# Kernel optimization log

Measured on AMD Instinct MI355X. Metric: run time of the kernel, lower is better.

The kernel has to match this reference:

```python
import jax, jax.numpy as jnp
import numpy as np

B, F, T, C, G = 2, 2048, 750, 20, 3
K = int(T * 0.125)  # top-k for score_pre


def _conv1d(x, w, b=None, pad=0):
    # x: (N, Cin, L), w: (Cout, Cin, k)
    out = jax.lax.conv_general_dilated(x, w, (1,), [(pad, pad)],
                                       dimension_numbers=('NCH', 'OIH', 'NCH'))
    return out if b is None else out + b[None, :, None]


def _base(x, w1, b1, w2, b2):
    # BaseModule: two k=3 convs with LeakyReLU(0.01); dropout = identity (eval)
    h = jax.nn.leaky_relu(_conv1d(x, w1, b1, pad=1))
    h = jax.nn.leaky_relu(_conv1d(h, w2, b2, pad=1))
    return h


def _post_cls(feat_agg, w1, b1, w2, b2, wc, batch, g):
    # feat_agg: (batch*C, F, g) -> BaseModule -> grouped 1x1 classifier -> mean over g
    h = _base(feat_agg, w1, b1, w2, b2)            # (batch*C, 2048, g)
    h = h.reshape(batch, C, 2048, g)
    score = jnp.einsum('bckg,ck->bcg', h, wc[:, :, 0])  # grouped conv1d, groups=C
    return score.mean(axis=2)                       # (batch, C)


def setup_inputs():
    key = jax.random.key(0)
    ks = jax.random.split(key, 8)
    s = 0.02
    x = jax.random.normal(ks[0], (B, F, T), jnp.float32)
    w1 = jax.random.normal(ks[1], (2048, F, 3), jnp.float32) * s
    b1 = jnp.zeros((2048,), jnp.float32)
    w2 = jax.random.normal(ks[2], (2048, 2048, 3), jnp.float32) * s
    b2 = jnp.zeros((2048,), jnp.float32)
    wc = jax.random.normal(ks[3], (C, 2048, 1), jnp.float32) * s   # classifier, no bias
    watt = jax.random.normal(ks[4], (C, C, 1), jnp.float32) * s    # attention 1x1 conv
    batt = jnp.zeros((C,), jnp.float32)
    cls_label = (jax.random.uniform(ks[5], (B, C)) < 0.15).astype(jnp.int32)
    cls_label = cls_label.at[:, 0].set(1)  # guarantee >=1 gt class per video
    return {'x': x, 'w1': w1, 'b1': b1, 'w2': w2, 'b2': b2, 'wc': wc,
            'watt': watt, 'batt': batt, 'cls_label': cls_label,
            'groups': G, 'is_train': 1}


def reference(x, w1, b1, w2, b2, wc, watt, batt, cls_label, groups, is_train):
    g = groups
    Tg = T // g
    seq_cas = _conv1d(_base(x, w1, b1, w2, b2), wc)           # (B, C, T)
    score_pre = jax.lax.top_k(seq_cas, K)[0].mean(axis=2)     # (B, C)
    wa = jax.nn.sigmoid(_conv1d(seq_cas, watt, batt))         # (B, C, T) attention weights

    # _agg_feature: strided slice t = j*g + i  <=>  reshape T -> (Tg, g), group idx last
    xg = x.reshape(B, F, Tg, g)
    wag = wa.reshape(B, C, Tg, g)
    feat_agg = jnp.einsum('bcjg,bfjg->bcfg', wag, xg).reshape(B * C, F, g)
    score_post = _post_cls(feat_agg, w1, b1, w2, b2, wc, B, g)  # (B, C)

    if is_train:
        # background stream, vectorized over (batch, suppressed class c) with masking
        wbg = (1.0 - wa).reshape(B, C, Tg, g)
        # tiny intermediate (B,C,C,Tg,g), then contract with features
        ww = jnp.einsum('bajg,bcjg->bcajg', wag, wbg)
        agg = jnp.einsum('bcajg,bfjg->bcafg', ww, xg).reshape(B * C * C, F, g)
        sc = _post_cls(agg, w1, b1, w2, b2, wc, B * C, g).reshape(B, C, C)  # [b, suppressed c, class a]
        m = cls_label.astype(score_post.dtype)                 # (B, C) multi-hot
        ngt = jnp.maximum(m.sum(axis=1, keepdims=True), 1.0)
        collect = jnp.einsum('bc,bca->ba', m, sc) / ngt        # mean over gt classes
        diag = jnp.diagonal(sc, axis1=1, axis2=2)              # sc[b, j, j]
        collect = jnp.where(m > 0, diag, collect)              # overwrite gt entries
        score_agg = jax.nn.softmax(jnp.concatenate([score_post, collect], axis=1), axis=1)
        return (score_pre, score_post, score_agg)
    else:
        return (jax.nn.softmax(score_pre, axis=1), seq_cas)
```

## Files before the change

kernel.cpp:

```cpp
#include <hip/hip_runtime.h>
#include <math.h>

namespace {
constexpr int kF = 2048;
constexpr int kT = 750;
constexpr int kC = 20;
constexpr int kTop = 93;
}

typedef __bf16 bf16x8 __attribute__((ext_vector_type(8)));
typedef float f32x4 __attribute__((ext_vector_type(4)));

__device__ __forceinline__ ushort f2bf(float f) {
  uint u = __builtin_bit_cast(uint, f);
  uint r = u + 0x7FFFu + ((u >> 16) & 1u);
  return (ushort)(r >> 16);
}
__device__ __forceinline__ float bf2f(ushort u) {
  return __builtin_bit_cast(float, ((uint)u) << 16);
}
__device__ __forceinline__ float leaky(float v) { return v > 0.f ? v : 0.01f * v; }

__device__ __forceinline__ void gload_lds16(const ushort* g, ushort* l) {
  __builtin_amdgcn_global_load_lds(
      (const __attribute__((address_space(1))) void*)g,
      (__attribute__((address_space(3))) void*)l, 16, 0, 0);
}

__global__ void build_list_kernel(const int* __restrict__ lbl,
                                  int4* __restrict__ meta, int* __restrict__ cnt) {
  if (threadIdx.x != 0) return;
  int n = 0;
  for (int b = 0; b < 2; ++b) {
    cnt[4 + b] = n;
    for (int c = 0; c < kC; ++c) { meta[n] = make_int4(b, c, c, 1); ++n; }
    int nb0 = n;
    for (int c = 0; c < kC; ++c)
      for (int a = 0; a < kC; ++a)
        if (lbl[b * kC + c] > 0 || c == a) { meta[n] = make_int4(b, c, a, 0); ++n; }
    cnt[6 + b] = (n - cnt[4 + b]);
    (void)nb0;
  }
  cnt[0] = n;
  cnt[1] = n * 3;
  cnt[2] = 1500;
  cnt[3] = 0;
}

__global__ __launch_bounds__(256) void convert_w_kernel(
    const float* __restrict__ w1, const float* __restrict__ w2,
    ushort* __restrict__ Wt1, ushort* __restrict__ Wt2,
    ushort* __restrict__ zpage) {
  const int co = blockIdx.x;
  const float* w = (blockIdx.y == 0) ? w1 : w2;
  ushort* Wt = (blockIdx.y == 0) ? Wt1 : Wt2;
  const int ci0 = threadIdx.x * 8;
  float v[24];
  const float4* p = (const float4*)(w + (size_t)co * 6144 + ci0 * 3);
#pragma unroll
  for (int s = 0; s < 6; ++s) {
    float4 f = p[s];
    v[s * 4 + 0] = f.x; v[s * 4 + 1] = f.y; v[s * 4 + 2] = f.z; v[s * 4 + 3] = f.w;
  }
#pragma unroll
  for (int tap = 0; tap < 3; ++tap) {
    ushort o[8];
#pragma unroll
    for (int j = 0; j < 8; ++j) o[j] = f2bf(v[j * 3 + tap]);
    ushort4 a = {o[0], o[1], o[2], o[3]}, b = {o[4], o[5], o[6], o[7]};
    ushort4* q = (ushort4*)(Wt + (size_t)tap * kF * kF + (size_t)co * kF + ci0);
    q[0] = a; q[1] = b;
  }
  if (blockIdx.x == 0 && blockIdx.y == 0) {
    ((float4*)zpage)[threadIdx.x] = (float4){0.f, 0.f, 0.f, 0.f};
  }
}

__global__ __launch_bounds__(256) void convert_kernel(
    const float* __restrict__ src, ushort* __restrict__ dst, int n) {
  int i = (blockIdx.x * 256 + threadIdx.x) * 4;
  if (i + 3 < n) {
    float4 f = *(const float4*)(src + i);
    ushort4 o;
    o.x = f2bf(f.x); o.y = f2bf(f.y); o.z = f2bf(f.z); o.w = f2bf(f.w);
    *(ushort4*)(dst + i) = o;
  } else {
    for (; i < n; ++i) dst[i] = f2bf(src[i]);
  }
}

__global__ __launch_bounds__(256) void transpose_kernel(
    const float* __restrict__ x, ushort* __restrict__ xTt) {
  __shared__ float tile[64][65];
  const int b = blockIdx.z;
  const int t0 = blockIdx.x * 64, f0 = blockIdx.y * 64;
  const int tx = threadIdx.x & 63, ty4 = threadIdx.x >> 6;
#pragma unroll
  for (int i = 0; i < 16; ++i) {
    int lf = ty4 + i * 4;
    int t = t0 + tx;
    tile[lf][tx] = (t < kT) ? x[((size_t)b * kF + f0 + lf) * kT + t] : 0.f;
  }
  __syncthreads();
#pragma unroll
  for (int i = 0; i < 16; ++i) {
    int lt = ty4 + i * 4;
    int t = t0 + lt;
    if (t < kT)
      xTt[(size_t)(b * kT + t) * kF + f0 + tx] = f2bf(tile[tx][lt]);
  }
}

__global__ __launch_bounds__(256) void xj_kernel(
    const float* __restrict__ x, ushort* __restrict__ xJ) {
  const int bid = blockIdx.x;
  const int b = bid >> 11, f = bid & 2047;
  __shared__ float buf[768];
  const float* xr = x + ((size_t)b * kF + f) * kT;
  for (int t = threadIdx.x; t < kT; t += 256) buf[t] = xr[t];
  __syncthreads();
  const int j = threadIdx.x;
#pragma unroll
  for (int g = 0; g < 3; ++g) {
    float v = (j < 250) ? buf[j * 3 + g] : 0.f;
    xJ[(((size_t)(b * 3 + g) * kF + f) << 8) + j] = f2bf(v);
  }
}

__global__ __launch_bounds__(256) void ww_build_kernel(
    const float* __restrict__ wab, const int4* __restrict__ meta,
    const int* __restrict__ cnt, ushort* __restrict__ W2) {
  const int bg = blockIdx.x;
  const int b = bg / 3, g = bg % 3;
  const int r0 = blockIdx.y * 32;
  const int nb = cnt[6 + b], boff = cnt[4 + b];
  if (r0 >= nb) return;
  __shared__ float ws[kC][256];
  for (int i = threadIdx.x; i < kC * 250; i += 256) {
    int c = i / 250, j = i % 250;
    ws[c][j] = wab[(size_t)(b * kC + c) * kT + j * 3 + g];
  }
  __syncthreads();
  ushort* Wb = W2 + (size_t)bg * 512 * 256;
  const int j = threadIdx.x;
  for (int rr = 0; rr < 32; ++rr) {
    int r = r0 + rr;
    if (r >= nb) break;
    int4 m = meta[boff + r];
    float v = 0.f;
    if (j < 250)
      v = m.w ? ws[m.y][j] : ws[m.z][j] * (1.f - ws[m.y][j]);
    Wb[(size_t)r * 256 + j] = f2bf(v);
  }
}

__global__ __launch_bounds__(256) void ww_gemm_kernel(
    const ushort* __restrict__ xJ, const ushort* __restrict__ W2,
    const int* __restrict__ cnt, ushort* __restrict__ FeatY) {
  const int bg = blockIdx.z;
  const int b = bg / 3, g = bg % 3;
  const int nb = cnt[6 + b], boff = cnt[4 + b];
  const int s0 = blockIdx.x * 128;
  if (s0 >= nb) return;
  __shared__ ushort sA[2][128 * 64];
  __shared__ ushort sB[2][128 * 64];
  const int tid = threadIdx.x;
  const int w = tid >> 6, lane = tid & 63;
  const int wm = w >> 1, wn = w & 1;
  const int f0 = blockIdx.y * 128;
  const ushort* A = xJ + ((size_t)bg * kF << 8);
  const ushort* Bp = W2 + (size_t)bg * 512 * 256;
  const int srow = lane >> 3;
  const int selem = ((lane & 7) ^ srow) * 8;
  f32x4 acc[4][4];
#pragma unroll
  for (int i = 0; i < 4; ++i)
#pragma unroll
    for (int j = 0; j < 4; ++j) acc[i][j] = (f32x4){0.f, 0.f, 0.f, 0.f};

  auto STAGE = [&](int buf, int kt) {
    const int kin = kt * 64;
#pragma unroll
    for (int i = 0; i < 4; ++i) {
      int r = (w * 4 + i) * 8 + srow;
      gload_lds16(A + (size_t)(f0 + r) * 256 + kin + selem,
                  &sA[buf][(w * 4 + i) * 512]);
    }
#pragma unroll
    for (int i = 0; i < 4; ++i) {
      int r = (w * 4 + i) * 8 + srow;
      gload_lds16(Bp + (size_t)(s0 + r) * 256 + kin + selem,
                  &sB[buf][(w * 4 + i) * 512]);
    }
  };

  STAGE(0, 0);
  asm volatile("s_waitcnt vmcnt(0)" ::: "memory");
  __builtin_amdgcn_s_barrier();

  int cur = 0;
  for (int kt = 0; kt < 4; ++kt) {
    if (kt + 1 < 4) STAGE(cur ^ 1, kt + 1);
#pragma unroll
    for (int ksub = 0; ksub < 2; ++ksub) {
      bf16x8 af[4], bfv[4];
      const int rlow = lane & 7;
#pragma unroll
      for (int fm = 0; fm < 4; ++fm) {
        int row = wm * 64 + fm * 16 + (lane & 15);
        int c16 = (ksub * 4 + (lane >> 4)) ^ rlow;
        af[fm] = *(const bf16x8*)&sA[cur][row * 64 + c16 * 8];
      }
#pragma unroll
      for (int fn = 0; fn < 4; ++fn) {
        int row = wn * 64 + fn * 16 + (lane & 15);
        int c16 = (ksub * 4 + (lane >> 4)) ^ rlow;
        bfv[fn] = *(const bf16x8*)&sB[cur][row * 64 + c16 * 8];
      }
#pragma unroll
      for (int fm = 0; fm < 4; ++fm)
#pragma unroll
        for (int fn = 0; fn < 4; ++fn)
          acc[fm][fn] = __builtin_amdgcn_mfma_f32_16x16x32_bf16(
              af[fm], bfv[fn], acc[fm][fn], 0, 0, 0);
    }
    asm volatile("s_waitcnt vmcnt(0)" ::: "memory");
    __builtin_amdgcn_s_barrier();
    cur ^= 1;
  }

#pragma unroll
  for (int fm = 0; fm < 4; ++fm) {
#pragma unroll
    for (int fn = 0; fn < 4; ++fn) {
      int s = s0 + wn * 64 + fn * 16 + (lane & 15);
      if (s >= nb) continue;
      int row = f0 + wm * 64 + fm * 16 + ((lane >> 4) << 2);
      ushort4 o;
      o.x = f2bf(acc[fm][fn][0]);
      o.y = f2bf(acc[fm][fn][1]);
      o.z = f2bf(acc[fm][fn][2]);
      o.w = f2bf(acc[fm][fn][3]);
      *(ushort4*)&FeatY[(size_t)((boff + s) * 3 + g) * kF + row] = o;
    }
  }
}

template <int L>
__global__ __launch_bounds__(512, 1) void gemm_conv_kernel(
    const ushort* __restrict__ A, const ushort* __restrict__ B,
    const ushort* __restrict__ zpage, ushort* __restrict__ Cpart,
    const int* __restrict__ ncp, int NP, int ktn_base, int ktrem) {
  extern __shared__ ushort lds[];
  const int nc = *ncp;
  const int tid = threadIdx.x;
  const int wid = tid >> 6, lane = tid & 63;
  const int wr = wid >> 2, wc = wid & 3;
  const int gx = gridDim.x, gy = gridDim.y;
  const int nwg = gx * gy * gridDim.z;
  const int h = blockIdx.x + gx * (blockIdx.y + gy * blockIdx.z);
  const int lgc = (h & 7) * (nwg >> 3) + (h >> 3);
  const int bx = lgc % gx;
  const int byz = lgc / gx;
  const int co0 = (byz % gy) * 256;
  const int col0 = bx * 256;
  if (col0 >= nc) return;
  const int z = byz / gy;
  const int kt0 = z * ktn_base + (z < ktrem ? z : ktrem);
  const int ktn = ktn_base + (z < ktrem ? 1 : 0);
  const int ktend = kt0 + ktn;

  const int pofs = lane >> 3;
  const int lin_s = (lane & 7) ^ pofs;
  const int mofs = 2 * pofs + (lin_s >> 2);
  const int qseg = (lin_s & 3) * 8;
  const int l15 = lane & 15;
  const int seg8 = ((((l15 & 1) << 2) + (lane >> 4)) ^ (l15 >> 1)) * 8;
  const int off_rl = (l15 >> 1) * 64 + seg8;

  f32x4 acc[8][4];
#pragma unroll
  for (int i = 0; i < 8; ++i)
#pragma unroll
    for (int j = 0; j < 4; ++j) acc[i][j] = (f32x4){0.f, 0.f, 0.f, 0.f};

  auto STAGE_A = [&](int buf, int kt) {
    const int tap = kt >> 6;
    const int kin = (kt & 63) * 32;
    const size_t abase = (size_t)tap * kF * kF + kin + qseg;
#pragma unroll
    for (int l = 0; l < 2; ++l) {
      int m = l * 128 + wid * 16 + mofs;
      gload_lds16(A + abase + (size_t)(co0 + m) * kF,
                  &lds[buf * 16384 + l * 4096 + wid * 512]);
    }
  };
  auto STAGE_B = [&](int buf, int kt) {
    const int tap = kt >> 6;
    const int kin = (kt & 63) * 32;
#pragma unroll
    for (int l = 0; l < 2; ++l) {
      int m = l * 128 + wid * 16 + mofs;
      int col = col0 + m;
      int t = col - (col / L) * L;
      int tt = t + tap - 1;
      const ushort* src = (col < nc && tt >= 0 && tt < L)
          ? B + (size_t)(col + tap - 1) * kF + kin + qseg
          : zpage + qseg;
      gload_lds16(src, &lds[buf * 16384 + 8192 + l * 4096 + wid * 512]);
    }
  };

  STAGE_A(kt0 & 3, kt0);           STAGE_B(kt0 & 3, kt0);
  STAGE_A((kt0 + 1) & 3, kt0 + 1); STAGE_B((kt0 + 1) & 3, kt0 + 1);
  STAGE_A((kt0 + 2) & 3, kt0 + 2); STAGE_B((kt0 + 2) & 3, kt0 + 2);
  asm volatile("s_waitcnt vmcnt(8)" ::: "memory");
  __builtin_amdgcn_s_barrier();
  __builtin_amdgcn_sched_barrier(0);

  for (int kt = kt0; kt < ktend; ++kt) {
    const int buf = kt & 3;
    const int ts = (kt + 3 < ktend) ? kt + 3 : ktend - 1;
    const int bufs = ts & 3;
    const ushort* bb = &lds[buf * 16384];
    bf16x8 bfv[4], af[4];
    STAGE_A(bufs, ts);
#pragma unroll
    for (int fn = 0; fn < 4; ++fn)
      bfv[fn] = *(const bf16x8*)&bb[8192 + wc * 2048 + fn * 512 + off_rl];
#pragma unroll
    for (int fm = 0; fm < 4; ++fm)
      af[fm] = *(const bf16x8*)&bb[wr * 4096 + fm * 512 + off_rl];
    asm volatile("s_waitcnt lgkmcnt(0)" ::: "memory");
    __builtin_amdgcn_sched_barrier(0);
    __builtin_amdgcn_s_setprio(1);
#pragma unroll
    for (int fm = 0; fm < 4; ++fm)
#pragma unroll
      for (int fn = 0; fn < 4; ++fn)
        acc[fm][fn] = __builtin_amdgcn_mfma_f32_16x16x32_bf16(
            af[fm], bfv[fn], acc[fm][fn], 0, 0, 0);
    __builtin_amdgcn_s_setprio(0);
    STAGE_B(bufs, ts);
#pragma unroll
    for (int fm = 0; fm < 4; ++fm)
      af[fm] = *(const bf16x8*)&bb[wr * 4096 + (fm + 4) * 512 + off_rl];
    asm volatile("s_waitcnt lgkmcnt(0)" ::: "memory");
    __builtin_amdgcn_sched_barrier(0);
    __builtin_amdgcn_s_setprio(1);
#pragma unroll
    for (int fm = 0; fm < 4; ++fm)
#pragma unroll
      for (int fn = 0; fn < 4; ++fn)
        acc[fm + 4][fn] = __builtin_amdgcn_mfma_f32_16x16x32_bf16(
            af[fm], bfv[fn], acc[fm + 4][fn], 0, 0, 0);
    __builtin_amdgcn_s_setprio(0);
    asm volatile("s_waitcnt vmcnt(8)" ::: "memory");
    __builtin_amdgcn_s_barrier();
    __builtin_amdgcn_sched_barrier(0);
  }

  ushort* Cz = Cpart + (size_t)z * NP * kF;
#pragma unroll
  for (int fm = 0; fm < 8; ++fm) {
#pragma unroll
    for (int fn = 0; fn < 4; ++fn) {
      int col = col0 + wc * 64 + fn * 16 + l15;
      int row = co0 + wr * 128 + fm * 16 + ((lane >> 4) << 2);
      ushort4 o;
      o.x = f2bf(acc[fm][fn][0]);
      o.y = f2bf(acc[fm][fn][1]);
      o.z = f2bf(acc[fm][fn][2]);
      o.w = f2bf(acc[fm][fn][3]);
      *(ushort4*)&Cz[(size_t)col * kF + row] = o;
    }
  }
}

__global__ __launch_bounds__(256) void reduce_kernel(
    const ushort* __restrict__ Cpart, const float* __restrict__ bias,
    ushort* __restrict__ Y, const int* __restrict__ ncp, int NP, int S) {
  const int col = blockIdx.x;
  if (col >= *ncp) return;
  const int row0 = threadIdx.x * 8;
  float s[8] = {};
  for (int z = 0; z < S; ++z) {
    const ushort* p = &Cpart[((size_t)z * NP + col) * kF + row0];
    ushort4 a = *(const ushort4*)p;
    ushort4 b = *(const ushort4*)(p + 4);
    s[0] += bf2f(a.x); s[1] += bf2f(a.y); s[2] += bf2f(a.z); s[3] += bf2f(a.w);
    s[4] += bf2f(b.x); s[5] += bf2f(b.y); s[6] += bf2f(b.z); s[7] += bf2f(b.w);
  }
  float4 bv0 = *(const float4*)&bias[row0];
  float4 bv1 = *(const float4*)&bias[row0 + 4];
  ushort4 o0, o1;
  o0.x = f2bf(leaky(s[0] + bv0.x)); o0.y = f2bf(leaky(s[1] + bv0.y));
  o0.z = f2bf(leaky(s[2] + bv0.z)); o0.w = f2bf(leaky(s[3] + bv0.w));
  o1.x = f2bf(leaky(s[4] + bv1.x)); o1.y = f2bf(leaky(s[5] + bv1.y));
  o1.z = f2bf(leaky(s[6] + bv1.z)); o1.w = f2bf(leaky(s[7] + bv1.w));
  *(ushort4*)&Y[(size_t)col * kF + row0] = o0;
  *(ushort4*)&Y[(size_t)col * kF + row0 + 4] = o1;
}

__global__ __launch_bounds__(256) void seqcas_kernel(
    const ushort* __restrict__ h2, const ushort* __restrict__ wcb,
    const float* __restrict__ watt, const float* __restrict__ batt,
    float* __restrict__ seq, float* __restrict__ wa) {
  const int w = threadIdx.x >> 6, lane = threadIdx.x & 63;
  const int idx = blockIdx.x * 4 + w;
  if (idx >= 2 * kT) return;
  const ushort* hr = h2 + (size_t)idx * kF;
  float acc[kC];
#pragma unroll
  for (int c = 0; c < kC; ++c) acc[c] = 0.f;
#pragma unroll
  for (int ch = 0; ch < 4; ++ch) {
    const int ci0 = ch * 512 + lane * 8;
    ushort4 ha = *(const ushort4*)(hr + ci0);
    ushort4 hb = *(const ushort4*)(hr + ci0 + 4);
    float hx[8] = {bf2f(ha.x), bf2f(ha.y), bf2f(ha.z), bf2f(ha.w),
                   bf2f(hb.x), bf2f(hb.y), bf2f(hb.z), bf2f(hb.w)};
#pragma unroll
    for (int c = 0; c < kC; ++c) {
      const ushort* wr = wcb + c * kF + ci0;
      ushort4 wa4 = *(const ushort4*)wr;
      ushort4 wb4 = *(const ushort4*)(wr + 4);
      acc[c] += bf2f(wa4.x) * hx[0] + bf2f(wa4.y) * hx[1] +
                bf2f(wa4.z) * hx[2] + bf2f(wa4.w) * hx[3] +
                bf2f(wb4.x) * hx[4] + bf2f(wb4.y) * hx[5] +
                bf2f(wb4.z) * hx[6] + bf2f(wb4.w) * hx[7];
    }
  }
#pragma unroll
  for (int off = 32; off; off >>= 1)
#pragma unroll
    for (int c = 0; c < kC; ++c) acc[c] += __shfl_xor(acc[c], off);
  if (lane == 0) {
    int b = idx / kT, t = idx % kT;
#pragma unroll
    for (int c = 0; c < kC; ++c) seq[(size_t)(b * kC + c) * kT + t] = acc[c];
#pragma unroll
    for (int c = 0; c < kC; ++c) {
      float z = batt[c];
#pragma unroll
      for (int a = 0; a < kC; ++a) z += watt[c * kC + a] * acc[a];
      wa[(size_t)(b * kC + c) * kT + t] = 1.f / (1.f + expf(-z));
    }
  }
}

__global__ __launch_bounds__(64) void score_pre_kernel(
    const float* __restrict__ seq, float* __restrict__ out) {
  const int n = blockIdx.x;
  const int lane = threadIdx.x;
  float v[12];
#pragma unroll
  for (int i = 0; i < 12; ++i) {
    int idx = lane + i * 64;
    v[i] = (idx < kT) ? seq[(size_t)n * kT + idx] : -1e30f;
  }
  float sum = 0.f;
  for (int it = 0; it < kTop; ++it) {
    float lm = v[0];
#pragma unroll
    for (int i = 1; i < 12; ++i) lm = fmaxf(lm, v[i]);
    float wm = lm;
#pragma unroll
    for (int off = 32; off; off >>= 1) wm = fmaxf(wm, __shfl_xor(wm, off));
    sum += wm;
    unsigned long long ball = __ballot(lm == wm);
    int first = __ffsll(ball) - 1;
    bool own = (lane == first);
    bool done = false;
#pragma unroll
    for (int i = 0; i < 12; ++i) {
      bool hit = own && !done && (v[i] == wm);
      if (hit) { v[i] = -1e30f; done = true; }
    }
  }
  if (lane == 0) out[n] = sum / (float)kTop;
}

__global__ __launch_bounds__(256) void cls_kernel(
    const ushort* __restrict__ h, const float* __restrict__ wc,
    const int4* __restrict__ meta, const int* __restrict__ cnt,
    float* __restrict__ out40, float* __restrict__ scb) {
  __shared__ float red[256];
  const int n = blockIdx.x;
  if (n >= cnt[0]) return;
  const int tid = threadIdx.x;
  const int4 m = meta[n];
  const int cls = m.w ? m.y : m.z;
  const int co0 = tid * 8;
  const float4 w0 = *(const float4*)(wc + (size_t)cls * kF + co0);
  const float4 w1 = *(const float4*)(wc + (size_t)cls * kF + co0 + 4);
  float acc = 0.f;
#pragma unroll
  for (int g = 0; g < 3; ++g) {
    const ushort* hr = h + (size_t)(n * 3 + g) * kF + co0;
    ushort4 a = *(const ushort4*)hr;
    ushort4 b4 = *(const ushort4*)(hr + 4);
    acc += bf2f(a.x) * w0.x + bf2f(a.y) * w0.y + bf2f(a.z) * w0.z + bf2f(a.w) * w0.w +
           bf2f(b4.x) * w1.x + bf2f(b4.y) * w1.y + bf2f(b4.z) * w1.z + bf2f(b4.w) * w1.w;
  }
  red[tid] = acc;
  __syncthreads();
  for (int s = 128; s > 0; s >>= 1) {
    if (tid < s) red[tid] += red[tid + s];
    __syncthreads();
  }
  if (tid == 0) {
    float v = red[0] * (1.f / 3.f);
    if (m.w) out40[m.x * kC + m.y];
    if (m.w) out40[m.x * kC + m.y] = v;
    else scb[m.x * 400 + m.y * kC + m.z] = v;
  }
}

__global__ void final_kernel(const float* __restrict__ score_post,
                             const float* __restrict__ sc_buf,
                             const int* __restrict__ label,
                             float* __restrict__ out) {
  __shared__ float z[2 * kC];
  __shared__ float collect[kC];
  const int b = blockIdx.x;
  const int tid = threadIdx.x;
  if (tid < kC) {
    int a = tid;
    float s = 0.f, ngt = 0.f;
    for (int c = 0; c < kC; ++c) {
      if (label[b * kC + c] > 0) {
        ngt += 1.f;
        s += sc_buf[b * 400 + c * kC + a];
      }
    }
    if (ngt < 1.f) ngt = 1.f;
    float col = s / ngt;
    if (label[b * kC + a] > 0) col = sc_buf[b * 400 + a * kC + a];
    collect[a] = col;
  }
  __syncthreads();
  if (tid < 2 * kC) z[tid] = (tid < kC) ? score_post[b * kC + tid] : collect[tid - kC];
  __syncthreads();
  if (tid == 0) {
    float mx = z[0];
    for (int i = 1; i < 2 * kC; ++i) mx = fmaxf(mx, z[i]);
    float s = 0.f;
    for (int i = 0; i < 2 * kC; ++i) { z[i] = expf(z[i] - mx); s += z[i]; }
    for (int i = 0; i < 2 * kC; ++i) out[80 + b * 2 * kC + i] = z[i] / s;
  }
}

extern "C" void kernel_launch(void* const* d_in, const int* in_sizes, int n_in,
                              void* d_out, int out_size, void* d_ws, size_t ws_size,
                              hipStream_t stream) {
  (void)in_sizes; (void)n_in; (void)out_size;
  const float* x    = (const float*)d_in[0];
  const float* w1   = (const float*)d_in[1];
  const float* b1   = (const float*)d_in[2];
  const float* w2   = (const float*)d_in[3];
  const float* b2   = (const float*)d_in[4];
  const float* wc   = (const float*)d_in[5];
  const float* watt = (const float*)d_in[6];
  const float* batt = (const float*)d_in[7];
  const int*   lbl  = (const int*)d_in[8];
  float* out = (float*)d_out;
  char*  wsb = (char*)d_ws;

  hipFuncSetAttribute(reinterpret_cast<const void*>(&gemm_conv_kernel<750>),
                      hipFuncAttributeMaxDynamicSharedMemorySize, 131072);
  hipFuncSetAttribute(reinterpret_cast<const void*>(&gemm_conv_kernel<3>),
                      hipFuncAttributeMaxDynamicSharedMemorySize, 131072);

  ushort* Wt1   = (ushort*)(wsb + 0);
  ushort* Wt2   = (ushort*)(wsb + 25165824);
  ushort* wcb   = (ushort*)(wsb + 50331648);
  ushort* zpage = (ushort*)(wsb + 50413568);
  ushort* xTt   = (ushort*)(wsb + 50417664);
  ushort* xJ    = (ushort*)(wsb + 56561664);
  ushort* W2b   = (ushort*)(wsb + 62853120);
  ushort* Ybuf  = (ushort*)(wsb + 64425984);
  ushort* h2    = (ushort*)(wsb + 74747904);
  ushort* hP2   = (ushort*)(wsb + 80891904);
  float*  seq   = (float*)(wsb + 91213824);
  float*  wab   = (float*)(wsb + 91333824);
  float*  scb   = (float*)(wsb + 91453824);
  int*    cnt   = (int*)(wsb + 91457024);
  int4*   meta  = (int4*)(wsb + 91457088);
  ushort* Ppart = (ushort*)(wsb + 91470848);

  const int S_main = 5;
  const size_t ppart_off = 91470848;
  const size_t avail = (ws_size > ppart_off) ? ws_size - ppart_off : 0;
  const int S_post = (avail >= (size_t)8 * 2560 * 2048 * 2) ? 8
                   : (avail >= (size_t)6 * 2560 * 2048 * 2) ? 6 : 4;
  const int ktn_post = 192 / S_post;

  dim3 blk(256);
  build_list_kernel<<<dim3(1), dim3(64), 0, stream>>>(lbl, meta, cnt);
  convert_w_kernel<<<dim3(2048, 2), blk, 0, stream>>>(w1, w2, Wt1, Wt2, zpage);
  convert_kernel<<<dim3(40), blk, 0, stream>>>(wc, wcb, kC * kF);
  transpose_kernel<<<dim3(12, 32, 2), blk, 0, stream>>>(x, xTt);
  xj_kernel<<<dim3(4096), blk, 0, stream>>>(x, xJ);
  gemm_conv_kernel<750><<<dim3(6, 8, S_main), dim3(512), 131072, stream>>>(
      Wt1, xTt, zpage, Ppart, &cnt[2], 1536, 38, 2);
  reduce_kernel<<<dim3(1500), blk, 0, stream>>>(Ppart, b1, Ybuf, &cnt[2], 1536, S_main);
  gemm_conv_kernel<750><<<dim3(6, 8, S_main), dim3(512), 131072, stream>>>(
      Wt2, Ybuf, zpage, Ppart, &cnt[2], 1536, 38, 2);
  reduce_kernel<<<dim3(1500), blk, 0, stream>>>(Ppart, b2, h2, &cnt[2], 1536, S_main);
  seqcas_kernel<<<dim3(375), blk, 0, stream>>>(h2, wcb, watt, batt, seq, wab);
  score_pre_kernel<<<dim3(40), dim3(64), 0, stream>>>(seq, out);
  ww_build_kernel<<<dim3(6, 16), blk, 0, stream>>>(wab, meta, cnt, W2b);
  ww_gemm_kernel<<<dim3(4, 16, 6), blk, 0, stream>>>(xJ, W2b, cnt, Ybuf);
  gemm_conv_kernel<3><<<dim3(10, 8, S_post), dim3(512), 131072, stream>>>(
      Wt1, Ybuf, zpage, Ppart, &cnt[1], 2560, ktn_post, 0);
  reduce_kernel<<<dim3(2520), blk, 0, stream>>>(Ppart, b1, Ybuf, &cnt[1], 2560, S_post);
  gemm_conv_kernel<3><<<dim3(10, 8, S_post), dim3(512), 131072, stream>>>(
      Wt2, Ybuf, zpage, Ppart, &cnt[1], 2560, ktn_post, 0);
  reduce_kernel<<<dim3(2520), blk, 0, stream>>>(Ppart, b2, hP2, &cnt[1], 2560, S_post);
  cls_kernel<<<dim3(840), blk, 0, stream>>>(hP2, wc, meta, cnt, out + 40, scb);
  final_kernel<<<dim3(2), dim3(64), 0, stream>>>(out + 40, scb, lbl, out);
}
```

Before: 354.0 us.

## Fuse final split-K reduce with classifier dot and merge GEMM inner-loop halves

The last split-K reduction now applies bias, LeakyReLU and bf16 rounding, then dots the result directly with the classifier weights. Per-column partial scores go to a small buffer and a tiny kernel averages over the three groups. This removes the write and re-read of the post-stage hidden activations. Separately, the GEMM inner loop now issues both global-to-LDS stages up front and loads all eight A fragments before one 32-MFMA burst, dropping an intermediate lgkmcnt wait. That raises register pressure and changes how loads interleave with the matrix ops.

```diff
diff --git a/kernel.cpp b/kernel.cpp
--- a/kernel.cpp
+++ b/kernel.cpp
@@ -34,12 +34,10 @@
   for (int b = 0; b < 2; ++b) {
     cnt[4 + b] = n;
     for (int c = 0; c < kC; ++c) { meta[n] = make_int4(b, c, c, 1); ++n; }
-    int nb0 = n;
     for (int c = 0; c < kC; ++c)
       for (int a = 0; a < kC; ++a)
         if (lbl[b * kC + c] > 0 || c == a) { meta[n] = make_int4(b, c, a, 0); ++n; }
     cnt[6 + b] = (n - cnt[4 + b]);
-    (void)nb0;
   }
   cnt[0] = n;
   cnt[1] = n * 3;
@@ -323,37 +321,22 @@
     const int ts = (kt + 3 < ktend) ? kt + 3 : ktend - 1;
     const int bufs = ts & 3;
     const ushort* bb = &lds[buf * 16384];
-    bf16x8 bfv[4], af[4];
     STAGE_A(bufs, ts);
+    STAGE_B(bufs, ts);
+    bf16x8 bfv[4], af[8];
 #pragma unroll
     for (int fn = 0; fn < 4; ++fn)
       bfv[fn] = *(const bf16x8*)&bb[8192 + wc * 2048 + fn * 512 + off_rl];
 #pragma unroll
-    for (int fm = 0; fm < 4; ++fm)
+    for (int fm = 0; fm < 8; ++fm)
       af[fm] = *(const bf16x8*)&bb[wr * 4096 + fm * 512 + off_rl];
-    asm volatile("s_waitcnt lgkmcnt(0)" ::: "memory");
-    __builtin_amdgcn_sched_barrier(0);
     __builtin_amdgcn_s_setprio(1);
 #pragma unroll
-    for (int fm = 0; fm < 4; ++fm)
+    for (int fm = 0; fm < 8; ++fm)
 #pragma unroll
       for (int fn = 0; fn < 4; ++fn)
         acc[fm][fn] = __builtin_amdgcn_mfma_f32_16x16x32_bf16(
             af[fm], bfv[fn], acc[fm][fn], 0, 0, 0);
-    __builtin_amdgcn_s_setprio(0);
-    STAGE_B(bufs, ts);
-#pragma unroll
-    for (int fm = 0; fm < 4; ++fm)
-      af[fm] = *(const bf16x8*)&bb[wr * 4096 + (fm + 4) * 512 + off_rl];
-    asm volatile("s_waitcnt lgkmcnt(0)" ::: "memory");
-    __builtin_amdgcn_sched_barrier(0);
-    __builtin_amdgcn_s_setprio(1);
-#pragma unroll
-    for (int fm = 0; fm < 4; ++fm)
-#pragma unroll
-      for (int fn = 0; fn < 4; ++fn)
-        acc[fm + 4][fn] = __builtin_amdgcn_mfma_f32_16x16x32_bf16(
-            af[fm], bfv[fn], acc[fm + 4][fn], 0, 0, 0);
     __builtin_amdgcn_s_setprio(0);
     asm volatile("s_waitcnt vmcnt(8)" ::: "memory");
     __builtin_amdgcn_s_barrier();
@@ -402,6 +385,54 @@
   *(ushort4*)&Y[(size_t)col * kF + row0 + 4] = o1;
 }
 
+__global__ __launch_bounds__(256) void reduce_cls_kernel(
+    const ushort* __restrict__ Cpart, const float* __restrict__ bias,
+    const float* __restrict__ wc, const int4* __restrict__ meta,
+    const int* __restrict__ cnt, float* __restrict__ scpart, int NP, int S) {
+  __shared__ float red[256];
+  const int col = blockIdx.x;
+  if (col >= cnt[1]) return;
+  const int4 m = meta[col / 3];
+  const int cls = m.w ? m.y : m.z;
+  const int row0 = threadIdx.x * 8;
+  float s[8] = {};
+  for (int z = 0; z < S; ++z) {
+    const ushort* p = &Cpart[((size_t)z * NP + col) * kF + row0];
+    ushort4 a = *(const ushort4*)p;
+    ushort4 b = *(const ushort4*)(p + 4);
+    s[0] += bf2f(a.x); s[1] += bf2f(a.y); s[2] += bf2f(a.z); s[3] += bf2f(a.w);
+    s[4] += bf2f(b.x); s[5] += bf2f(b.y); s[6] += bf2f(b.z); s[7] += bf2f(b.w);
+  }
+  float4 bv0 = *(const float4*)&bias[row0];
+  float4 bv1 = *(const float4*)&bias[row0 + 4];
+  float4 w0 = *(const float4*)&wc[(size_t)cls * kF + row0];
+  float4 w1 = *(const float4*)&wc[(size_t)cls * kF + row0 + 4];
+  float acc =
+      bf2f(f2bf(leaky(s[0] + bv0.x))) * w0.x + bf2f(f2bf(leaky(s[1] + bv0.y))) * w0.y +
+      bf2f(f2bf(leaky(s[2] + bv0.z))) * w0.z + bf2f(f2bf(leaky(s[3] + bv0.w))) * w0.w +
+      bf2f(f2bf(leaky(s[4] + bv1.x))) * w1.x + bf2f(f2bf(leaky(s[5] + bv1.y))) * w1.y +
+      bf2f(f2bf(leaky(s[6] + bv1.z))) * w1.z + bf2f(f2bf(leaky(s[7] + bv1.w))) * w1.w;
+  red[threadIdx.x] = acc;
+  __syncthreads();
+  for (int t = 128; t > 0; t >>= 1) {
+    if (threadIdx.x < t) red[threadIdx.x] += red[threadIdx.x + t];
+    __syncthreads();
+  }
+  if (threadIdx.x == 0) scpart[col] = red[0];
+}
+
+__global__ __launch_bounds__(256) void cls2_kernel(
+    const float* __restrict__ scpart, const int4* __restrict__ meta,
+    const int* __restrict__ cnt, float* __restrict__ out40,
+    float* __restrict__ scb) {
+  const int n = blockIdx.x * 256 + threadIdx.x;
+  if (n >= cnt[0]) return;
+  const int4 m = meta[n];
+  float v = (scpart[3 * n] + scpart[3 * n + 1] + scpart[3 * n + 2]) * (1.f / 3.f);
+  if (m.w) out40[m.x * kC + m.y] = v;
+  else scb[m.x * 400 + m.y * kC + m.z] = v;
+}
+
 __global__ __launch_bounds__(256) void seqcas_kernel(
     const ushort* __restrict__ h2, const ushort* __restrict__ wcb,
     const float* __restrict__ watt, const float* __restrict__ batt,
@@ -479,42 +510,6 @@
     }
   }
   if (lane == 0) out[n] = sum / (float)kTop;
-}
-
-__global__ __launch_bounds__(256) void cls_kernel(
-    const ushort* __restrict__ h, const float* __restrict__ wc,
-    const int4* __restrict__ meta, const int* __restrict__ cnt,
-    float* __restrict__ out40, float* __restrict__ scb) {
-  __shared__ float red[256];
-  const int n = blockIdx.x;
-  if (n >= cnt[0]) return;
-  const int tid = threadIdx.x;
-  const int4 m = meta[n];
-  const int cls = m.w ? m.y : m.z;
-  const int co0 = tid * 8;
-  const float4 w0 = *(const float4*)(wc + (size_t)cls * kF + co0);
-  const float4 w1 = *(const float4*)(wc + (size_t)cls * kF + co0 + 4);
-  float acc = 0.f;
-#pragma unroll
-  for (int g = 0; g < 3; ++g) {
-    const ushort* hr = h + (size_t)(n * 3 + g) * kF + co0;
-    ushort4 a = *(const ushort4*)hr;
-    ushort4 b4 = *(const ushort4*)(hr + 4);
-    acc += bf2f(a.x) * w0.x + bf2f(a.y) * w0.y + bf2f(a.z) * w0.z + bf2f(a.w) * w0.w +
-           bf2f(b4.x) * w1.x + bf2f(b4.y) * w1.y + bf2f(b4.z) * w1.z + bf2f(b4.w) * w1.w;
-  }
-  red[tid] = acc;
-  __syncthreads();
-  for (int s = 128; s > 0; s >>= 1) {
-    if (tid < s) red[tid] += red[tid + s];
-    __syncthreads();
-  }
-  if (tid == 0) {
-    float v = red[0] * (1.f / 3.f);
-    if (m.w) out40[m.x * kC + m.y];
-    if (m.w) out40[m.x * kC + m.y] = v;
-    else scb[m.x * 400 + m.y * kC + m.z] = v;
-  }
 }
 
 __global__ void final_kernel(const float* __restrict__ score_post,
@@ -581,7 +576,7 @@
   ushort* W2b   = (ushort*)(wsb + 62853120);
   ushort* Ybuf  = (ushort*)(wsb + 64425984);
   ushort* h2    = (ushort*)(wsb + 74747904);
-  ushort* hP2   = (ushort*)(wsb + 80891904);
+  float*  scpart= (float*)(wsb + 80891904);
   float*  seq   = (float*)(wsb + 91213824);
   float*  wab   = (float*)(wsb + 91333824);
   float*  scb   = (float*)(wsb + 91453824);
@@ -617,7 +612,8 @@
   reduce_kernel<<<dim3(2520), blk, 0, stream>>>(Ppart, b1, Ybuf, &cnt[1], 2560, S_post);
   gemm_conv_kernel<3><<<dim3(10, 8, S_post), dim3(512), 131072, stream>>>(
       Wt2, Ybuf, zpage, Ppart, &cnt[1], 2560, ktn_post, 0);
-  reduce_kernel<<<dim3(2520), blk, 0, stream>>>(Ppart, b2, hP2, &cnt[1], 2560, S_post);
-  cls_kernel<<<dim3(840), blk, 0, stream>>>(hP2, wc, meta, cnt, out + 40, scb);
+  reduce_cls_kernel<<<dim3(2520), blk, 0, stream>>>(
+      Ppart, b2, wc, meta, cnt, scpart, 2560, S_post);
+  cls2_kernel<<<dim3(4), blk, 0, stream>>>(scpart, meta, cnt, out + 40, scb);
   final_kernel<<<dim3(2), dim3(64), 0, stream>>>(out + 40, scb, lbl, out);
 }
```

Measured after the change: 358.0 us. Within noise of the previous version (+1.1%).
